# Performance work log

Hardware: AMD Instinct MI355X
Metric: run time of the kernel (lower is better)

## Reference

```python
import jax, jax.numpy as jnp
import numpy as np

MG = (5, 5)          # mesh_grid_size
UP = (17, 17)        # upsample_size
IMG = (512.0, 512.0) # image_size
B = 8192
FC_OUT = MG[0] * MG[1] * 2  # 50
KH = (UP[0] - 1) // (MG[0] - 1) + 1  # 5
KW = (UP[1] - 1) // (MG[1] - 1) + 1  # 5
SH = (UP[0] - 1) // (MG[0] - 1)      # 4
SW = (UP[1] - 1) // (MG[1] - 1)      # 4
L0 = MG[0] - 1
L1 = MG[1] - 1


def _grid(h, w):
    # channel 0: x coords vary along rows (image_size[0]); channel 1: y along cols
    x_t = jnp.broadcast_to(jnp.linspace(0.0, IMG[0], h)[:, None], (h, w))
    y_t = jnp.broadcast_to(jnp.linspace(0.0, IMG[1], w)[None, :], (h, w))
    return jnp.stack([x_t, y_t], 0)  # [2, h, w]


def _unfold22(a):
    # a: [B, 2, H, W] -> [B, (H-1)*(W-1), 4, 2]; 4 = kernel positions row-major, 2 = channel
    p = jnp.stack([a[:, :, :-1, :-1], a[:, :, :-1, 1:],
                   a[:, :, 1:, :-1], a[:, :, 1:, 1:]], axis=2)  # [B,2,4,H-1,W-1]
    return p.reshape(a.shape[0], 2, 4, -1).transpose(0, 3, 2, 1)


def _persp(src, dst):
    # exact 4-point homography solve (torchgeometry.get_perspective_transform)
    x0, y0 = src[..., 0], src[..., 1]
    u, v = dst[..., 0], dst[..., 1]
    z = jnp.zeros_like(x0)
    o = jnp.ones_like(x0)
    ax = jnp.stack([x0, y0, o, z, z, z, -u * x0, -u * y0], -1)  # [N,4,8]
    ay = jnp.stack([z, z, z, x0, y0, o, -v * x0, -v * y0], -1)
    A = jnp.concatenate([ax, ay], 1)                 # [N,8,8]
    bb = jnp.concatenate([u, v], 1)[..., None]       # [N,8,1]
    h = jnp.linalg.solve(A, bb)[..., 0]              # [N,8]
    return jnp.concatenate([h, o[:, :1]], 1).reshape(-1, 3, 3)


def setup_inputs() -> dict:
    key = jax.random.key(0)
    ks = jax.random.split(key, 4)
    def lin(k, i, o):
        return jax.random.normal(k, (i, o), jnp.float32) / jnp.sqrt(i)
    return {
        "x": jax.random.normal(ks[0], (B, 1024), jnp.float32),
        "W1": lin(ks[1], 1024, 1024), "b1": jnp.zeros((1024,), jnp.float32),
        "W2": lin(ks[2], 1024, 2048), "b2": jnp.zeros((2048,), jnp.float32),
        "W3": lin(ks[3], 2048, FC_OUT), "b3": jnp.zeros((FC_OUT,), jnp.float32),
    }


def reference(x, W1, b1, W2, b2, W3, b3):
    Bn = x.shape[0]
    h = jax.nn.relu(x @ W1 + b1)
    h = jax.nn.relu(h @ W2 + b2)
    out = (h @ W3 + b3).reshape(Bn, 2, MG[0], MG[1])  # [B,2,5,5] mesh flow

    # sparse control grid and 2x2 patch corner points
    gs = _grid(MG[0], MG[1])
    src = _unfold22(jnp.broadcast_to(gs[None], (Bn, 2, MG[0], MG[1]))).reshape(-1, 4, 2)
    flow = _unfold22(out).reshape(-1, 4, 2)
    M = _persp(src, src + flow)  # [B*16, 3, 3]

    # dense grid and its unfold2 (kernel KHxKW, stride SHxSW) patch points
    gd = _grid(UP[0], UP[1])  # [2, 17, 17]
    gi = (np.arange(L0) * SH)[:, None, None, None] + np.arange(KH)[None, None, :, None]
    gj = (np.arange(L1) * SW)[None, :, None, None] + np.arange(KW)[None, None, None, :]
    I, J = np.broadcast_arrays(gi, gj)  # [L0,L1,KH,KW]
    pts = gd[:, I, J].transpose(1, 2, 3, 4, 0).reshape(1, L0 * L1, KH * KW, 2)
    pts = jnp.broadcast_to(pts, (Bn, L0 * L1, KH * KW, 2)).reshape(Bn * L0 * L1, KH * KW, 2)

    # transform_points: homogeneous warp + perspective divide
    ph = jnp.concatenate([pts, jnp.ones(pts.shape[:-1] + (1,), pts.dtype)], -1)
    oh = jnp.einsum('nij,npj->npi', M, ph)
    warped = oh[..., :2] / oh[..., 2:3]
    warped = warped.reshape(Bn, L0, L1, KH, KW, 2)

    # Fold: scatter-accumulate overlapping patches
    fold = jnp.zeros((Bn, 2, UP[0], UP[1]), x.dtype)
    for i in range(L0):
        for j in range(L1):
            blk = warped[:, i, j].transpose(0, 3, 1, 2)  # [B,2,KH,KW]
            fold = fold.at[:, :, i * SH:i * SH + KH, j * SW:j * SW + KW].add(blk)

    # boundary rescaling exactly as the torch code: only the 5x5 crossing points
    idx = np.arange(0, UP[0], MG[0] - 1)
    X, Y = np.meshgrid(idx, idx, indexing='xy')
    fold = fold.at[:, :, X, Y].multiply(0.5)
    for (a, b) in ((0, 0), (0, UP[1] - 1), (UP[0] - 1, UP[1] - 1), (UP[0] - 1, 0)):
        fold = fold.at[:, :, a, b].multiply(2.0)

    return fold - gd[None]  # upsampled mesh flow [B,2,17,17]
```

## Files before the change

### kernel.cpp

```cpp
#include <hip/hip_runtime.h>

typedef __bf16 bf16x8 __attribute__((ext_vector_type(8)));
typedef float f32x4 __attribute__((ext_vector_type(4)));

__device__ __forceinline__ unsigned short f2bf(float f) {
  unsigned int u = __builtin_bit_cast(unsigned int, f);
  unsigned int r = (u + 0x7fffu + ((u >> 16) & 1u)) >> 16;
  return (unsigned short)r;
}

__device__ __forceinline__ float bf2f(unsigned short u) {
  unsigned int v = ((unsigned int)u) << 16;
  return __builtin_bit_cast(float, v);
}

__device__ __forceinline__ void load16_lds(const unsigned short* g, unsigned short* l) {
  __builtin_amdgcn_global_load_lds(
      (const __attribute__((address_space(1))) void*)g,
      (__attribute__((address_space(3))) void*)l, 16, 0, 0);
}

__device__ __forceinline__ void wait_vm0() {
  asm volatile("s_waitcnt vmcnt(0)" ::: "memory");
  __builtin_amdgcn_sched_barrier(0);
}
__device__ __forceinline__ void barrier_raw() {
  __builtin_amdgcn_sched_barrier(0);
  __builtin_amdgcn_s_barrier();
  __builtin_amdgcn_sched_barrier(0);
}


__global__ __launch_bounds__(256) void prepass(
    const float* __restrict__ x, const float* __restrict__ W1,
    const float* __restrict__ W2, const float* __restrict__ W3,
    unsigned short* __restrict__ xbf, unsigned short* __restrict__ w1t,
    unsigned short* __restrict__ w2t, unsigned short* __restrict__ w3t) {
  __shared__ float tile[32][33];
  const int bid = blockIdx.x;
  const int t = threadIdx.x;
  if (bid < 2048) {
    for (int i = bid * 256 + t; i < 2097152; i += 2048 * 256) {
      float4 f = ((const float4*)x)[i];
      uint2 o;
      o.x = (unsigned)f2bf(f.x) | ((unsigned)f2bf(f.y) << 16);
      o.y = (unsigned)f2bf(f.z) | ((unsigned)f2bf(f.w) << 16);
      ((uint2*)xbf)[i] = o;
    }
  } else if (bid < 3072) {
    int ti = bid - 2048;
    int n0 = (ti & 31) * 32, k0 = (ti >> 5) * 32;
    int tx = t & 31, ty = t >> 5;
    #pragma unroll
    for (int r = 0; r < 32; r += 8)
      tile[ty + r][tx] = W1[(size_t)(k0 + ty + r) * 1024 + n0 + tx];
    __syncthreads();
    #pragma unroll
    for (int r = 0; r < 32; r += 8)
      w1t[(size_t)(n0 + ty + r) * 1024 + k0 + tx] = f2bf(tile[tx][ty + r]);
  } else if (bid < 5120) {
    int ti = bid - 3072;
    int n0 = (ti & 63) * 32, k0 = (ti >> 6) * 32;
    int tx = t & 31, ty = t >> 5;
    #pragma unroll
    for (int r = 0; r < 32; r += 8)
      tile[ty + r][tx] = W2[(size_t)(k0 + ty + r) * 2048 + n0 + tx];
    __syncthreads();
    #pragma unroll
    for (int r = 0; r < 32; r += 8)
      w2t[(size_t)(n0 + ty + r) * 1024 + k0 + tx] = f2bf(tile[tx][ty + r]);
  } else {
    int idx = (bid - 5120) * 256 + t;
    int n = idx >> 11, k = idx & 2047;
    w3t[idx] = f2bf((n < 50) ? W3[(size_t)k * 50 + n] : 0.f);
  }
}


__global__ __launch_bounds__(512, 2) void gemm1_8p(
    const unsigned short* __restrict__ A,
    const unsigned short* __restrict__ Bt,
    const float* __restrict__ bias,
    unsigned short* __restrict__ C) {
  constexpr int K = 1024, N = 1024, NT = 16;
  constexpr int AEL = 256 * 64;
  constexpr int BEL = 128 * 64;
  constexpr int BUF = AEL + BEL;
  __shared__ __align__(16) unsigned short smem[2 * BUF];
  const int t = threadIdx.x;
  const int m0 = blockIdx.x * 256;
  const int n0 = blockIdx.y * 128;
  const int lane = t & 63, wv = t >> 6;
  const int l16 = lane & 15, quad = lane >> 4;
  const int rb = (wv >> 1) * 64, cb = (wv & 1) * 64;

  const int srow = t >> 3;
  const int sg = ((t & 7) ^ (srow & 7)) * 8;
  const unsigned short* Ag0 = A + (size_t)(m0 + srow) * K + sg;
  const unsigned short* Bg0 = Bt + (size_t)(n0 + srow) * K + sg;
  const int ldsO = wv * 8 * 64;

  f32x4 acc[4][4] = {};

  #pragma unroll
  for (int r = 0; r < 4; ++r)
    load16_lds(Ag0 + (size_t)(r * 64) * K, &smem[r * 4096 + ldsO]);
  #pragma unroll
  for (int r = 0; r < 2; ++r)
    load16_lds(Bg0 + (size_t)(r * 64) * K, &smem[AEL + r * 4096 + ldsO]);

  for (int kt = 0; kt < NT; ++kt) {
    unsigned short* Ls = &smem[(kt & 1) * BUF];

    wait_vm0();
    barrier_raw();

    if (kt + 1 < NT) {
      unsigned short* Ln = &smem[((kt + 1) & 1) * BUF];
      const unsigned short* An = Ag0 + (size_t)(kt + 1) * 64;
      const unsigned short* Bn = Bg0 + (size_t)(kt + 1) * 64;
      #pragma unroll
      for (int r = 0; r < 4; ++r)
        load16_lds(An + (size_t)(r * 64) * K, &Ln[r * 4096 + ldsO]);
      #pragma unroll
      for (int r = 0; r < 2; ++r)
        load16_lds(Bn + (size_t)(r * 64) * K, &Ln[AEL + r * 4096 + ldsO]);
    }

    #pragma unroll
    for (int half = 0; half < 2; ++half) {
      bf16x8 af[4], bfr[4];
      #pragma unroll
      for (int ni = 0; ni < 4; ++ni) {
        int row = cb + ni * 16 + l16;
        bfr[ni] = *(const bf16x8*)&Ls[AEL + row * 64 + ((half * 4 + quad) ^ (row & 7)) * 8];
      }
      #pragma unroll
      for (int mi = 0; mi < 4; ++mi) {
        int row = rb + mi * 16 + l16;
        af[mi] = *(const bf16x8*)&Ls[row * 64 + ((half * 4 + quad) ^ (row & 7)) * 8];
      }
      #pragma unroll
      for (int mi = 0; mi < 4; ++mi)
        #pragma unroll
        for (int ni = 0; ni < 4; ++ni)
          acc[mi][ni] = __builtin_amdgcn_mfma_f32_16x16x32_bf16(
              af[mi], bfr[ni], acc[mi][ni], 0, 0, 0);
    }
  }
  barrier_raw();

  unsigned short* Cs = smem;
  float bv[4];
  #pragma unroll
  for (int ni = 0; ni < 4; ++ni) bv[ni] = bias[n0 + cb + ni * 16 + l16];
  #pragma unroll
  for (int mi = 0; mi < 4; ++mi)
    #pragma unroll
    for (int ni = 0; ni < 4; ++ni)
      #pragma unroll
      for (int r = 0; r < 4; ++r) {
        int row = rb + mi * 16 + quad * 4 + r;
        int col = cb + ni * 16 + l16;
        int pb = (col >> 3) ^ (row & 15);
        Cs[row * 128 + pb * 8 + (col & 7)] = f2bf(fmaxf(acc[mi][ni][r] + bv[ni], 0.f));
      }
  __syncthreads();
  #pragma unroll
  for (int j = 0; j < 8; ++j) {
    int idx = j * 512 + t;
    int row = idx >> 4, cg = idx & 15;
    int pb = cg ^ (row & 15);
    *(uint4*)&C[(size_t)(m0 + row) * N + n0 + cg * 8] =
        *(const uint4*)&Cs[row * 128 + pb * 8];
  }
}


__global__ __launch_bounds__(512, 2) void gemm2_8p(
    const unsigned short* __restrict__ A,
    const unsigned short* __restrict__ Bt,
    const float* __restrict__ bias,
    const unsigned short* __restrict__ W3t,
    unsigned short* __restrict__ part) {
  constexpr int K = 1024, NT = 16;
  constexpr int AEL = 256 * 64;
  constexpr int BUF = 2 * AEL;
  __shared__ __align__(16) unsigned short smem[2 * BUF];
  const int t = threadIdx.x;
  const int m0 = blockIdx.x * 256;
  const int n0 = blockIdx.y * 256;
  const int lane = t & 63, wv = t >> 6;
  const int l16 = lane & 15, quad = lane >> 4;
  const int rb = (wv >> 2) * 128, cb = (wv & 3) * 64;

  const int srow = t >> 3;
  const int sg = ((t & 7) ^ (srow & 7)) * 8;
  const unsigned short* Ag0 = A + (size_t)(m0 + srow) * K + sg;
  const unsigned short* Bg0 = Bt + (size_t)(n0 + srow) * K + sg;
  const int ldsO = wv * 8 * 64;

  f32x4 acc[8][4] = {};

  #pragma unroll
  for (int r = 0; r < 4; ++r) {
    load16_lds(Ag0 + (size_t)(r * 64) * K, &smem[r * 4096 + ldsO]);
    load16_lds(Bg0 + (size_t)(r * 64) * K, &smem[AEL + r * 4096 + ldsO]);
  }

  for (int kt = 0; kt < NT; ++kt) {
    unsigned short* Ls = &smem[(kt & 1) * BUF];

    wait_vm0();
    barrier_raw();

    if (kt + 1 < NT) {
      unsigned short* Ln = &smem[((kt + 1) & 1) * BUF];
      const unsigned short* An = Ag0 + (size_t)(kt + 1) * 64;
      const unsigned short* Bn = Bg0 + (size_t)(kt + 1) * 64;
      #pragma unroll
      for (int r = 0; r < 4; ++r) {
        load16_lds(An + (size_t)(r * 64) * K, &Ln[r * 4096 + ldsO]);
        load16_lds(Bn + (size_t)(r * 64) * K, &Ln[AEL + r * 4096 + ldsO]);
      }
    }

    #pragma unroll
    for (int half = 0; half < 2; ++half) {
      bf16x8 bfr[4];
      #pragma unroll
      for (int ni = 0; ni < 4; ++ni) {
        int row = cb + ni * 16 + l16;
        bfr[ni] = *(const bf16x8*)&Ls[AEL + row * 64 + ((half * 4 + quad) ^ (row & 7)) * 8];
      }
      bf16x8 af[8];
      #pragma unroll
      for (int mi = 0; mi < 8; ++mi) {
        int row = rb + mi * 16 + l16;
        af[mi] = *(const bf16x8*)&Ls[row * 64 + ((half * 4 + quad) ^ (row & 7)) * 8];
      }
      #pragma unroll
      for (int mi = 0; mi < 8; ++mi)
        #pragma unroll
        for (int ni = 0; ni < 4; ++ni)
          acc[mi][ni] = __builtin_amdgcn_mfma_f32_16x16x32_bf16(
              af[mi], bfr[ni], acc[mi][ni], 0, 0, 0);
    }
  }
  barrier_raw();

  unsigned short* Cs = smem;
  float bv[4];
  #pragma unroll
  for (int ni = 0; ni < 4; ++ni) bv[ni] = bias[n0 + cb + ni * 16 + l16];
  #pragma unroll
  for (int mi = 0; mi < 8; ++mi)
    #pragma unroll
    for (int ni = 0; ni < 4; ++ni)
      #pragma unroll
      for (int r = 0; r < 4; ++r) {
        int row = rb + mi * 16 + quad * 4 + r;
        int col = cb + ni * 16 + l16;
        int pb = (col >> 3) ^ (row & 31);
        Cs[row * 256 + pb * 8 + (col & 7)] = f2bf(fmaxf(acc[mi][ni][r] + bv[ni], 0.f));
      }
  __syncthreads();

  bf16x8 bq[8][4];
  #pragma unroll
  for (int ks = 0; ks < 8; ++ks)
    #pragma unroll
    for (int nt = 0; nt < 4; ++nt)
      bq[ks][nt] = *(const bf16x8*)&W3t[(size_t)(nt * 16 + l16) * 2048 +
                                        n0 + ks * 32 + quad * 8];
  f32x4 acc2[2][4] = {};
  #pragma unroll
  for (int ks = 0; ks < 8; ++ks) {
    bf16x8 af2[2];
    #pragma unroll
    for (int mt = 0; mt < 2; ++mt) {
      int row = wv * 32 + mt * 16 + l16;
      int pb = (ks * 4 + quad) ^ (row & 31);
      af2[mt] = *(const bf16x8*)&Cs[row * 256 + pb * 8];
    }
    #pragma unroll
    for (int mt = 0; mt < 2; ++mt)
      #pragma unroll
      for (int nt = 0; nt < 4; ++nt)
        acc2[mt][nt] = __builtin_amdgcn_mfma_f32_16x16x32_bf16(
            af2[mt], bq[ks][nt], acc2[mt][nt], 0, 0, 0);
  }

  const int zi = blockIdx.y;
  #pragma unroll
  for (int mt = 0; mt < 2; ++mt)
    #pragma unroll
    for (int nt = 0; nt < 4; ++nt) {
      int col = nt * 16 + l16;
      #pragma unroll
      for (int r = 0; r < 4; ++r) {
        int row = m0 + wv * 32 + mt * 16 + quad * 4 + r;
        part[((size_t)row * 8 + zi) * 64 + col] = f2bf(acc2[mt][nt][r]);
      }
    }
}


__global__ __launch_bounds__(256) void geom_reduce(
    const unsigned short* __restrict__ part,
    const float* __restrict__ b3,
    float* __restrict__ outp) {
  __shared__ float s_out3[16 * 64];
  __shared__ float unfold[16][16][50];
  const int t = threadIdx.x;
  const int bbase = blockIdx.x * 16;

  for (int i = t; i < 1024; i += 256) {
    int m = i >> 6, n = i & 63;
    const unsigned short* p = part + ((size_t)(bbase + m) * 8) * 64 + n;
    float v = 0.f;
    #pragma unroll
    for (int z = 0; z < 8; ++z) v += bf2f(p[z * 64]);
    s_out3[i] = v + ((n < 50) ? b3[n] : 0.f);
  }
  __syncthreads();

  {
    const int bl = t >> 4;
    const int p = t & 15;
    const int pi = p >> 2, pj = p & 3;
    const float* o = &s_out3[bl * 64];

    float u00 = 128.f * pi       + o[pi * 5 + pj];
    float v00 = 128.f * pj       + o[25 + pi * 5 + pj];
    float u01 = 128.f * pi       + o[pi * 5 + pj + 1];
    float v01 = 128.f * (pj + 1) + o[25 + pi * 5 + pj + 1];
    float u10 = 128.f * (pi + 1) + o[(pi + 1) * 5 + pj];
    float v10 = 128.f * pj       + o[25 + (pi + 1) * 5 + pj];
    float u11 = 128.f * (pi + 1) + o[(pi + 1) * 5 + pj + 1];
    float v11 = 128.f * (pj + 1) + o[25 + (pi + 1) * 5 + pj + 1];

    float sx = u00 - u10 + u11 - u01;
    float sy = v00 - v10 + v11 - v01;
    float dx1 = u10 - u11, dx2 = u01 - u11;
    float dy1 = v10 - v11, dy2 = v01 - v11;
    float rden = 1.f / (dx1 * dy2 - dx2 * dy1);
    float g = (sx * dy2 - dx2 * sy) * rden;
    float h = (dx1 * sy - sx * dy1) * rden;
    float a = u10 - u00 + g * u10;
    float b = u01 - u00 + h * u01;
    float c = u00;
    float d = v10 - v00 + g * v10;
    float e = v01 - v00 + h * v01;
    float f = v00;

    #pragma unroll
    for (int ai = 0; ai < 5; ++ai) {
      #pragma unroll
      for (int bi = 0; bi < 5; ++bi) {
        float s = 0.25f * ai, tt = 0.25f * bi;
        float rw = 1.f / (g * s + h * tt + 1.f);
        unfold[bl][p][ai * 5 + bi]      = (a * s + b * tt + c) * rw;
        unfold[bl][p][25 + ai * 5 + bi] = (d * s + e * tt + f) * rw;
      }
    }
  }
  __syncthreads();

  for (int i = t; i < 16 * 578; i += 256) {
    int blb = i / 578;
    int rem = i - blb * 578;
    int ch = rem / 289;
    int ij = rem - ch * 289;
    int gi = ij / 17, gj = ij - gi * 17;

    int pi0 = (gi == 16) ? 3 : (gi >> 2);
    int ai0 = gi - 4 * pi0;
    int ci = (((gi & 3) == 0) && gi != 0 && gi != 16) ? 2 : 1;
    int pj0 = (gj == 16) ? 3 : (gj >> 2);
    int bj0 = gj - 4 * pj0;
    int cj = (((gj & 3) == 0) && gj != 0 && gj != 16) ? 2 : 1;

    float val = 0.f;
    #pragma unroll
    for (int ii = 0; ii < 2; ++ii) {
      if (ii < ci) {
        int pi = pi0 - ii, ai = ii ? 4 : ai0;
        #pragma unroll
        for (int jj = 0; jj < 2; ++jj) {
          if (jj < cj) {
            int pj = pj0 - jj, bi = jj ? 4 : bj0;
            val += unfold[blb][pi * 4 + pj][ch * 25 + ai * 5 + bi];
          }
        }
      }
    }

    if (((gi & 3) == 0) && ((gj & 3) == 0)) val *= 0.5f;
    if ((gi == 0 || gi == 16) && (gj == 0 || gj == 16)) val *= 2.f;
    val -= (ch == 0) ? 32.f * gi : 32.f * gj;
    outp[(size_t)(bbase + blb) * 578 + rem] = val;
  }
}


extern "C" void kernel_launch(void* const* d_in, const int* in_sizes, int n_in,
                              void* d_out, int out_size, void* d_ws, size_t ws_size,
                              hipStream_t stream) {
  const float* x  = (const float*)d_in[0];
  const float* W1 = (const float*)d_in[1];
  const float* b1 = (const float*)d_in[2];
  const float* W2 = (const float*)d_in[3];
  const float* b2 = (const float*)d_in[4];
  const float* W3 = (const float*)d_in[5];
  const float* b3 = (const float*)d_in[6];
  float* outp = (float*)d_out;

  char* ws = (char*)d_ws;
  unsigned short* xbf = (unsigned short*)ws;
  unsigned short* w1t = (unsigned short*)(ws + (size_t)16 * 1024 * 1024);
  unsigned short* part = (unsigned short*)ws;
  unsigned short* w2t = (unsigned short*)(ws + (size_t)34 * 1024 * 1024);
  unsigned short* w3t = (unsigned short*)(ws + (size_t)38 * 1024 * 1024);
  unsigned short* h1  = (unsigned short*)(ws + (size_t)38 * 1024 * 1024 + 512 * 1024);

  prepass<<<5632, 256, 0, stream>>>(x, W1, W2, W3, xbf, w1t, w2t, w3t);

  gemm1_8p<<<dim3(32, 8), 512, 0, stream>>>(xbf, w1t, b1, h1);
  gemm2_8p<<<dim3(32, 8), 512, 0, stream>>>(h1, w2t, b2, w3t, part);
  geom_reduce<<<512, 256, 0, stream>>>(part, b3, outp);
}
```

Before: 177.0 us.

## Retile both GEMMs into smaller blocks to raise grid size and occupancy

GEMM1 drops from 256x128 tiles with 512 threads to 128x128 tiles with 256 threads, doubling the grid. GEMM2 moves from 256x256 tiles with 64-wide K steps to 256x128 tiles with 32-wide K steps, a new rotation-based LDS swizzle, smaller LDS and a 4-blocks-per-CU launch bound. GEMM2's fused W3 projection now writes 16 partial slices instead of 8, so the reduce kernel sums 16 partials. The aim is better CU utilisation and latency hiding, at the cost of less data reuse per tile, more global loads and more partial-sum traffic.

```diff
diff --git a/kernel.cpp b/kernel.cpp
--- a/kernel.cpp
+++ b/kernel.cpp
@@ -77,16 +77,114 @@
 }
 
 
-__global__ __launch_bounds__(512, 2) void gemm1_8p(
+__global__ __launch_bounds__(256, 2) void gemm1_v8(
     const unsigned short* __restrict__ A,
     const unsigned short* __restrict__ Bt,
     const float* __restrict__ bias,
     unsigned short* __restrict__ C) {
   constexpr int K = 1024, N = 1024, NT = 16;
-  constexpr int AEL = 256 * 64;
-  constexpr int BEL = 128 * 64;
+  constexpr int AEL = 128 * 64;
+  constexpr int BUF = 2 * AEL;
+  __shared__ __align__(16) unsigned short smem[2 * BUF];
+  const int t = threadIdx.x;
+  const int m0 = blockIdx.x * 128;
+  const int n0 = blockIdx.y * 128;
+  const int lane = t & 63, wv = t >> 6;
+  const int l16 = lane & 15, quad = lane >> 4;
+  const int rb = (wv >> 1) * 64, cb = (wv & 1) * 64;
+
+  const int srow = t >> 3;
+  const int sg = ((t & 7) ^ (srow & 7)) * 8;
+  const unsigned short* Ag0 = A + (size_t)(m0 + srow) * K + sg;
+  const unsigned short* Bg0 = Bt + (size_t)(n0 + srow) * K + sg;
+  const int ldsO = wv * 8 * 64;
+
+  f32x4 acc[4][4] = {};
+
+  #pragma unroll
+  for (int r = 0; r < 4; ++r) {
+    load16_lds(Ag0 + (size_t)(r * 32) * K, &smem[r * 2048 + ldsO]);
+    load16_lds(Bg0 + (size_t)(r * 32) * K, &smem[AEL + r * 2048 + ldsO]);
+  }
+
+  for (int kt = 0; kt < NT; ++kt) {
+    unsigned short* Ls = &smem[(kt & 1) * BUF];
+
+    wait_vm0();
+    barrier_raw();
+
+    if (kt + 1 < NT) {
+      unsigned short* Ln = &smem[((kt + 1) & 1) * BUF];
+      const unsigned short* An = Ag0 + (size_t)(kt + 1) * 64;
+      const unsigned short* Bn = Bg0 + (size_t)(kt + 1) * 64;
+      #pragma unroll
+      for (int r = 0; r < 4; ++r) {
+        load16_lds(An + (size_t)(r * 32) * K, &Ln[r * 2048 + ldsO]);
+        load16_lds(Bn + (size_t)(r * 32) * K, &Ln[AEL + r * 2048 + ldsO]);
+      }
+    }
+
+    #pragma unroll
+    for (int half = 0; half < 2; ++half) {
+      bf16x8 af[4], bfr[4];
+      #pragma unroll
+      for (int ni = 0; ni < 4; ++ni) {
+        int row = cb + ni * 16 + l16;
+        bfr[ni] = *(const bf16x8*)&Ls[AEL + row * 64 + ((half * 4 + quad) ^ (row & 7)) * 8];
+      }
+      #pragma unroll
+      for (int mi = 0; mi < 4; ++mi) {
+        int row = rb + mi * 16 + l16;
+        af[mi] = *(const bf16x8*)&Ls[row * 64 + ((half * 4 + quad) ^ (row & 7)) * 8];
+      }
+      #pragma unroll
+      for (int mi = 0; mi < 4; ++mi)
+        #pragma unroll
+        for (int ni = 0; ni < 4; ++ni)
+          acc[mi][ni] = __builtin_amdgcn_mfma_f32_16x16x32_bf16(
+              af[mi], bfr[ni], acc[mi][ni], 0, 0, 0);
+    }
+  }
+  barrier_raw();
+
+  unsigned short* Cs = smem;
+  float bv[4];
+  #pragma unroll
+  for (int ni = 0; ni < 4; ++ni) bv[ni] = bias[n0 + cb + ni * 16 + l16];
+  #pragma unroll
+  for (int mi = 0; mi < 4; ++mi)
+    #pragma unroll
+    for (int ni = 0; ni < 4; ++ni)
+      #pragma unroll
+      for (int r = 0; r < 4; ++r) {
+        int row = rb + mi * 16 + quad * 4 + r;
+        int col = cb + ni * 16 + l16;
+        int pb = (col >> 3) ^ (row & 15);
+        Cs[row * 128 + pb * 8 + (col & 7)] = f2bf(fmaxf(acc[mi][ni][r] + bv[ni], 0.f));
+      }
+  __syncthreads();
+  #pragma unroll
+  for (int j = 0; j < 8; ++j) {
+    int idx = j * 256 + t;
+    int row = idx >> 4, cg = idx & 15;
+    int pb = cg ^ (row & 15);
+    *(uint4*)&C[(size_t)(m0 + row) * N + n0 + cg * 8] =
+        *(const uint4*)&Cs[row * 128 + pb * 8];
+  }
+}
+
+
+__global__ __launch_bounds__(512, 4) void gemm2_v8(
+    const unsigned short* __restrict__ A,
+    const unsigned short* __restrict__ Bt,
+    const float* __restrict__ bias,
+    const unsigned short* __restrict__ W3t,
+    unsigned short* __restrict__ part) {
+  constexpr int K = 1024, NT = 32;
+  constexpr int AEL = 256 * 32;
+  constexpr int BEL = 128 * 32;
   constexpr int BUF = AEL + BEL;
-  __shared__ __align__(16) unsigned short smem[2 * BUF];
+  __shared__ __align__(16) unsigned short smem[32768];
   const int t = threadIdx.x;
   const int m0 = blockIdx.x * 256;
   const int n0 = blockIdx.y * 128;
@@ -94,20 +192,17 @@
   const int l16 = lane & 15, quad = lane >> 4;
   const int rb = (wv >> 1) * 64, cb = (wv & 1) * 64;
 
-  const int srow = t >> 3;
-  const int sg = ((t & 7) ^ (srow & 7)) * 8;
-  const unsigned short* Ag0 = A + (size_t)(m0 + srow) * K + sg;
-  const unsigned short* Bg0 = Bt + (size_t)(n0 + srow) * K + sg;
-  const int ldsO = wv * 8 * 64;
+  const int tr = t >> 2;
+  const int cg = ((t & 3) - (tr >> 1)) & 3;
+  const unsigned short* Ag0 = A + (size_t)(m0 + tr) * K + cg * 8;
+  const unsigned short* Bg0 = Bt + (size_t)(n0 + tr) * K + cg * 8;
+  const int ldsO = wv * 512;
 
   f32x4 acc[4][4] = {};
 
-  #pragma unroll
-  for (int r = 0; r < 4; ++r)
-    load16_lds(Ag0 + (size_t)(r * 64) * K, &smem[r * 4096 + ldsO]);
-  #pragma unroll
-  for (int r = 0; r < 2; ++r)
-    load16_lds(Bg0 + (size_t)(r * 64) * K, &smem[AEL + r * 4096 + ldsO]);
+  load16_lds(Ag0, &smem[ldsO]);
+  load16_lds(Ag0 + (size_t)128 * K, &smem[4096 + ldsO]);
+  load16_lds(Bg0, &smem[AEL + ldsO]);
 
   for (int kt = 0; kt < NT; ++kt) {
     unsigned short* Ls = &smem[(kt & 1) * BUF];
@@ -117,36 +212,30 @@
 
     if (kt + 1 < NT) {
       unsigned short* Ln = &smem[((kt + 1) & 1) * BUF];
-      const unsigned short* An = Ag0 + (size_t)(kt + 1) * 64;
-      const unsigned short* Bn = Bg0 + (size_t)(kt + 1) * 64;
-      #pragma unroll
-      for (int r = 0; r < 4; ++r)
-        load16_lds(An + (size_t)(r * 64) * K, &Ln[r * 4096 + ldsO]);
-      #pragma unroll
-      for (int r = 0; r < 2; ++r)
-        load16_lds(Bn + (size_t)(r * 64) * K, &Ln[AEL + r * 4096 + ldsO]);
-    }
-
-    #pragma unroll
-    for (int half = 0; half < 2; ++half) {
-      bf16x8 af[4], bfr[4];
-      #pragma unroll
-      for (int ni = 0; ni < 4; ++ni) {
-        int row = cb + ni * 16 + l16;
-        bfr[ni] = *(const bf16x8*)&Ls[AEL + row * 64 + ((half * 4 + quad) ^ (row & 7)) * 8];
-      }
-      #pragma unroll
-      for (int mi = 0; mi < 4; ++mi) {
-        int row = rb + mi * 16 + l16;
-        af[mi] = *(const bf16x8*)&Ls[row * 64 + ((half * 4 + quad) ^ (row & 7)) * 8];
-      }
-      #pragma unroll
-      for (int mi = 0; mi < 4; ++mi)
-        #pragma unroll
-        for (int ni = 0; ni < 4; ++ni)
-          acc[mi][ni] = __builtin_amdgcn_mfma_f32_16x16x32_bf16(
-              af[mi], bfr[ni], acc[mi][ni], 0, 0, 0);
-    }
+      const unsigned short* An = Ag0 + (size_t)(kt + 1) * 32;
+      const unsigned short* Bn = Bg0 + (size_t)(kt + 1) * 32;
+      load16_lds(An, &Ln[ldsO]);
+      load16_lds(An + (size_t)128 * K, &Ln[4096 + ldsO]);
+      load16_lds(Bn, &Ln[AEL + ldsO]);
+    }
+
+    bf16x8 af[4], bfr[4];
+    #pragma unroll
+    for (int ni = 0; ni < 4; ++ni) {
+      int row = cb + ni * 16 + l16;
+      bfr[ni] = *(const bf16x8*)&Ls[AEL + row * 32 + ((quad + (row >> 1)) & 3) * 8];
+    }
+    #pragma unroll
+    for (int mi = 0; mi < 4; ++mi) {
+      int row = rb + mi * 16 + l16;
+      af[mi] = *(const bf16x8*)&Ls[row * 32 + ((quad + (row >> 1)) & 3) * 8];
+    }
+    #pragma unroll
+    for (int mi = 0; mi < 4; ++mi)
+      #pragma unroll
+      for (int ni = 0; ni < 4; ++ni)
+        acc[mi][ni] = __builtin_amdgcn_mfma_f32_16x16x32_bf16(
+            af[mi], bfr[ni], acc[mi][ni], 0, 0, 0);
   }
   barrier_raw();
 
@@ -166,122 +255,23 @@
         Cs[row * 128 + pb * 8 + (col & 7)] = f2bf(fmaxf(acc[mi][ni][r] + bv[ni], 0.f));
       }
   __syncthreads();
-  #pragma unroll
-  for (int j = 0; j < 8; ++j) {
-    int idx = j * 512 + t;
-    int row = idx >> 4, cg = idx & 15;
-    int pb = cg ^ (row & 15);
-    *(uint4*)&C[(size_t)(m0 + row) * N + n0 + cg * 8] =
-        *(const uint4*)&Cs[row * 128 + pb * 8];
-  }
-}
-
-
-__global__ __launch_bounds__(512, 2) void gemm2_8p(
-    const unsigned short* __restrict__ A,
-    const unsigned short* __restrict__ Bt,
-    const float* __restrict__ bias,
-    const unsigned short* __restrict__ W3t,
-    unsigned short* __restrict__ part) {
-  constexpr int K = 1024, NT = 16;
-  constexpr int AEL = 256 * 64;
-  constexpr int BUF = 2 * AEL;
-  __shared__ __align__(16) unsigned short smem[2 * BUF];
-  const int t = threadIdx.x;
-  const int m0 = blockIdx.x * 256;
-  const int n0 = blockIdx.y * 256;
-  const int lane = t & 63, wv = t >> 6;
-  const int l16 = lane & 15, quad = lane >> 4;
-  const int rb = (wv >> 2) * 128, cb = (wv & 3) * 64;
-
-  const int srow = t >> 3;
-  const int sg = ((t & 7) ^ (srow & 7)) * 8;
-  const unsigned short* Ag0 = A + (size_t)(m0 + srow) * K + sg;
-  const unsigned short* Bg0 = Bt + (size_t)(n0 + srow) * K + sg;
-  const int ldsO = wv * 8 * 64;
-
-  f32x4 acc[8][4] = {};
-
-  #pragma unroll
-  for (int r = 0; r < 4; ++r) {
-    load16_lds(Ag0 + (size_t)(r * 64) * K, &smem[r * 4096 + ldsO]);
-    load16_lds(Bg0 + (size_t)(r * 64) * K, &smem[AEL + r * 4096 + ldsO]);
-  }
-
-  for (int kt = 0; kt < NT; ++kt) {
-    unsigned short* Ls = &smem[(kt & 1) * BUF];
-
-    wait_vm0();
-    barrier_raw();
-
-    if (kt + 1 < NT) {
-      unsigned short* Ln = &smem[((kt + 1) & 1) * BUF];
-      const unsigned short* An = Ag0 + (size_t)(kt + 1) * 64;
-      const unsigned short* Bn = Bg0 + (size_t)(kt + 1) * 64;
-      #pragma unroll
-      for (int r = 0; r < 4; ++r) {
-        load16_lds(An + (size_t)(r * 64) * K, &Ln[r * 4096 + ldsO]);
-        load16_lds(Bn + (size_t)(r * 64) * K, &Ln[AEL + r * 4096 + ldsO]);
-      }
-    }
-
-    #pragma unroll
-    for (int half = 0; half < 2; ++half) {
-      bf16x8 bfr[4];
-      #pragma unroll
-      for (int ni = 0; ni < 4; ++ni) {
-        int row = cb + ni * 16 + l16;
-        bfr[ni] = *(const bf16x8*)&Ls[AEL + row * 64 + ((half * 4 + quad) ^ (row & 7)) * 8];
-      }
-      bf16x8 af[8];
-      #pragma unroll
-      for (int mi = 0; mi < 8; ++mi) {
-        int row = rb + mi * 16 + l16;
-        af[mi] = *(const bf16x8*)&Ls[row * 64 + ((half * 4 + quad) ^ (row & 7)) * 8];
-      }
-      #pragma unroll
-      for (int mi = 0; mi < 8; ++mi)
-        #pragma unroll
-        for (int ni = 0; ni < 4; ++ni)
-          acc[mi][ni] = __builtin_amdgcn_mfma_f32_16x16x32_bf16(
-              af[mi], bfr[ni], acc[mi][ni], 0, 0, 0);
-    }
-  }
-  barrier_raw();
-
-  unsigned short* Cs = smem;
-  float bv[4];
-  #pragma unroll
-  for (int ni = 0; ni < 4; ++ni) bv[ni] = bias[n0 + cb + ni * 16 + l16];
-  #pragma unroll
-  for (int mi = 0; mi < 8; ++mi)
-    #pragma unroll
-    for (int ni = 0; ni < 4; ++ni)
-      #pragma unroll
-      for (int r = 0; r < 4; ++r) {
-        int row = rb + mi * 16 + quad * 4 + r;
-        int col = cb + ni * 16 + l16;
-        int pb = (col >> 3) ^ (row & 31);
-        Cs[row * 256 + pb * 8 + (col & 7)] = f2bf(fmaxf(acc[mi][ni][r] + bv[ni], 0.f));
-      }
-  __syncthreads();
-
-  bf16x8 bq[8][4];
-  #pragma unroll
-  for (int ks = 0; ks < 8; ++ks)
+
+  bf16x8 bq[4][4];
+  #pragma unroll
+  for (int ks = 0; ks < 4; ++ks)
     #pragma unroll
     for (int nt = 0; nt < 4; ++nt)
       bq[ks][nt] = *(const bf16x8*)&W3t[(size_t)(nt * 16 + l16) * 2048 +
                                         n0 + ks * 32 + quad * 8];
   f32x4 acc2[2][4] = {};
   #pragma unroll
-  for (int ks = 0; ks < 8; ++ks) {
+  for (int ks = 0; ks < 4; ++ks) {
     bf16x8 af2[2];
     #pragma unroll
     for (int mt = 0; mt < 2; ++mt) {
       int row = wv * 32 + mt * 16 + l16;
-      int pb = (ks * 4 + quad) ^ (row & 31);
-      af2[mt] = *(const bf16x8*)&Cs[row * 256 + pb * 8];
+      int pb = (ks * 4 + quad) ^ (row & 15);
+      af2[mt] = *(const bf16x8*)&Cs[row * 128 + pb * 8];
     }
     #pragma unroll
     for (int mt = 0; mt < 2; ++mt)
@@ -300,7 +290,7 @@
       #pragma unroll
       for (int r = 0; r < 4; ++r) {
         int row = m0 + wv * 32 + mt * 16 + quad * 4 + r;
-        part[((size_t)row * 8 + zi) * 64 + col] = f2bf(acc2[mt][nt][r]);
+        part[((size_t)row * 16 + zi) * 64 + col] = f2bf(acc2[mt][nt][r]);
       }
     }
 }
@@ -317,10 +307,10 @@
 
   for (int i = t; i < 1024; i += 256) {
     int m = i >> 6, n = i & 63;
-    const unsigned short* p = part + ((size_t)(bbase + m) * 8) * 64 + n;
+    const unsigned short* p = part + ((size_t)(bbase + m) * 16) * 64 + n;
     float v = 0.f;
     #pragma unroll
-    for (int z = 0; z < 8; ++z) v += bf2f(p[z * 64]);
+    for (int z = 0; z < 16; ++z) v += bf2f(p[z * 64]);
     s_out3[i] = v + ((n < 50) ? b3[n] : 0.f);
   }
   __syncthreads();
@@ -426,7 +416,7 @@
 
   prepass<<<5632, 256, 0, stream>>>(x, W1, W2, W3, xbf, w1t, w2t, w3t);
 
-  gemm1_8p<<<dim3(32, 8), 512, 0, stream>>>(xbf, w1t, b1, h1);
-  gemm2_8p<<<dim3(32, 8), 512, 0, stream>>>(h1, w2t, b2, w3t, part);
+  gemm1_v8<<<dim3(64, 8), 256, 0, stream>>>(xbf, w1t, b1, h1);
+  gemm2_v8<<<dim3(32, 16), 512, 0, stream>>>(h1, w2t, b2, w3t, part);
   geom_reduce<<<512, 256, 0, stream>>>(part, b3, outp);
 }
```

Measured after the change: 184.1 us. 4.0% more time.
